# Kernel tuning notes

Hardware: AMD Instinct MI355X
Metric: run time of the kernel (lower is better)

The kernel has to match this reference:

```python
import jax, jax.numpy as jnp
import numpy as np

BLOCK = 128      # ModelArgs.block_size
FP8_MAX = 448.0  # e4m3 max, used by act_quant


def setup_inputs() -> dict:
    key = jax.random.key(0)
    k1, k2, k3 = jax.random.split(key, 3)
    M, K, O = 8192, 4096, 4096
    x = jax.random.normal(k1, (M, K), dtype=jnp.float32)
    # 'fp8' weight values (simulated in fp32) and blockwise fp32 scales
    weight = jax.random.normal(k2, (O, K), dtype=jnp.float32)
    w_scale = jax.random.uniform(k3, (O // BLOCK, K // BLOCK), dtype=jnp.float32,
                                 minval=0.5, maxval=1.5)
    return {"x": x, "weight": weight, "w_scale": w_scale}


def reference(x, weight, w_scale):
    M, K = x.shape
    O = weight.shape[0]
    Kb, Ob = K // BLOCK, O // BLOCK

    # --- act_quant: per-(row, k-block) scale = amax/448, quantized vals x/scale ---
    xb = x.reshape(M, Kb, BLOCK)
    sx = jnp.max(jnp.abs(xb), axis=-1, keepdims=True) / FP8_MAX  # [M, Kb, 1]
    xq = xb / sx                                                  # simulated fp8 activations

    # --- weight_dequant: blockwise scale expansion ---
    wdq = (weight.reshape(Ob, BLOCK, Kb, BLOCK) * w_scale[:, None, :, None]).reshape(O, K)

    # --- fp8_gemm: y = (xq * sx) @ wdq^T  (activation scales folded back per block) ---
    xd = (xq * sx).reshape(M, K)
    y = jnp.einsum('mk,ok->mo', xd, wdq)  # [M, O]
    return y
```

## Files before the change

### kernel.cpp

```cpp
#include <hip/hip_runtime.h>

#define M_DIM 8192
#define K_DIM 4096
#define O_DIM 4096
#define QB    128
#define BK    64
#define BMT   256
#define BNT   256

typedef __attribute__((ext_vector_type(8))) short  short8;
typedef __attribute__((ext_vector_type(4))) float  floatx4;

#define AS1 __attribute__((address_space(1)))
#define AS3 __attribute__((address_space(3)))

__device__ __forceinline__ short f2bf(float f) {
    unsigned u = __float_as_uint(f);
    unsigned r = u + 0x7fffu + ((u >> 16) & 1u);
    return (short)(r >> 16);
}

__global__ __launch_bounds__(512) void cvt_fused(const float* __restrict__ x,
                                                 const float* __restrict__ w,
                                                 const float* __restrict__ s,
                                                 short* __restrict__ xb,
                                                 short* __restrict__ wb) {
    const size_t NX = (size_t)M_DIM * K_DIM / 8;
    size_t t = (size_t)blockIdx.x * 512 + threadIdx.x;
    if (t < NX) {
        size_t i = t * 8;
        floatx4 f0 = *(const floatx4*)(x + i);
        floatx4 f1 = *(const floatx4*)(x + i + 4);
        short8 o;
        o[0] = f2bf(f0[0]); o[1] = f2bf(f0[1]); o[2] = f2bf(f0[2]); o[3] = f2bf(f0[3]);
        o[4] = f2bf(f1[0]); o[5] = f2bf(f1[1]); o[6] = f2bf(f1[2]); o[7] = f2bf(f1[3]);
        *(short8*)(xb + i) = o;
    } else {
        size_t i = (t - NX) * 8;
        int o = (int)(i >> 12);
        int k = (int)(i & (K_DIM - 1));
        float sc = s[(o >> 7) * (K_DIM / QB) + (k >> 7)];
        floatx4 f0 = *(const floatx4*)(w + i);
        floatx4 f1 = *(const floatx4*)(w + i + 4);
        short8 v;
        v[0] = f2bf(f0[0] * sc); v[1] = f2bf(f0[1] * sc);
        v[2] = f2bf(f0[2] * sc); v[3] = f2bf(f0[3] * sc);
        v[4] = f2bf(f1[0] * sc); v[5] = f2bf(f1[1] * sc);
        v[6] = f2bf(f1[2] * sc); v[7] = f2bf(f1[3] * sc);
        *(short8*)(wb + i) = v;
    }
}

#define WLG12 asm volatile("s_waitcnt lgkmcnt(12)" ::: "memory")
#define WLG8  asm volatile("s_waitcnt lgkmcnt(8)" ::: "memory")
#define WLG0  asm volatile("s_waitcnt lgkmcnt(0)" ::: "memory")
#define WVM2  asm volatile("s_waitcnt vmcnt(2)" ::: "memory")
#define WVM0  asm volatile("s_waitcnt vmcnt(0)" ::: "memory")
#define BARR  __builtin_amdgcn_s_barrier()
#define SCHEDB __builtin_amdgcn_sched_barrier(0)
#define SP1   __builtin_amdgcn_s_setprio(1)
#define SP0   __builtin_amdgcn_s_setprio(0)

#define LDA4(DST, BUF, ROFF)                                                    \
    _Pragma("unroll")                                                           \
    for (int mi = 0; mi < 4; ++mi) {                                            \
        DST[mi][0] = *(const short8*)&lsA[BUF][rA + (ROFF) + mi * 1024 + pc0];  \
        DST[mi][1] = *(const short8*)&lsA[BUF][rA + (ROFF) + mi * 1024 + pc1];  \
    }

#define LDB2(DST, BUF, ROFF)                                                    \
    _Pragma("unroll")                                                           \
    for (int ni = 0; ni < 2; ++ni) {                                            \
        DST[ni][0] = *(const short8*)&lsB[BUF][rB + (ROFF) + ni * 1024 + pc0];  \
        DST[ni][1] = *(const short8*)&lsB[BUF][rB + (ROFF) + ni * 1024 + pc1];  \
    }

#define RDA0(B) LDA4(a0, B, 0)
#define RDA1(B) LDA4(a1, B, 4096)
#define RDB0(B) LDB2(b0, B, 0)
#define RDB1(B) LDB2(b1, B, 2048)

#define MM16(AF, BF, MO, NO)                                                    \
    _Pragma("unroll")                                                           \
    for (int mi = 0; mi < 4; ++mi)                                              \
        _Pragma("unroll")                                                       \
        for (int ni = 0; ni < 2; ++ni)                                          \
            _Pragma("unroll")                                                   \
            for (int ks = 0; ks < 2; ++ks)                                      \
                acc[(MO) + mi][(NO) + ni] = __builtin_amdgcn_mfma_f32_16x16x32_bf16( \
                    AF[mi][ks], BF[ni][ks], acc[(MO) + mi][(NO) + ni], 0, 0, 0);

#define STAGE(LS, BUF, GP, KOFF, H)                                             \
    __builtin_amdgcn_global_load_lds(                                           \
        (const AS1 void*)((GP) + (size_t)((H) * 128) * K_DIM + (KOFF)),         \
        (AS3 void*)&LS[BUF][(H) * 128 * BK + dst], 16, 0, 0);                   \
    __builtin_amdgcn_global_load_lds(                                           \
        (const AS1 void*)((GP) + (size_t)((H) * 128 + 64) * K_DIM + (KOFF)),    \
        (AS3 void*)&LS[BUF][((H) * 128 + 64) * BK + dst], 16, 0, 0);

#define PH(STAGES, WAITM, MFMAS)                                                \
    STAGES                                                                      \
    BARR; WAITM; SCHEDB;                                                        \
    SP1;                                                                        \
    MFMAS                                                                       \
    SP0;                                                                        \
    BARR; SCHEDB;

#define PH3(STAGES, VMW, READS, MFMAS)                                          \
    STAGES                                                                      \
    VMW; BARR; SCHEDB;                                                          \
    READS                                                                       \
    WLG12; SCHEDB;                                                              \
    SP1;                                                                        \
    MFMAS                                                                       \
    SP0;                                                                        \
    BARR; SCHEDB;

#define TILE(c, n, k1, k2)                                                      \
    RDB1(c); RDA1(c);                                                           \
    PH(STAGE(lsA, n, gA, k1, 1), WLG12, MM16(a0, b0, 0, 0))                     \
    PH(STAGE(lsB, n, gB, k1, 0), WLG8,  MM16(a0, b1, 0, 2))                     \
    PH(STAGE(lsB, n, gB, k1, 1), WLG0,  MM16(a1, b0, 4, 0))                     \
    PH3(STAGE(lsA, c, gA, k2, 0), WVM2, RDA0(n); RDB0(n);, MM16(a1, b1, 4, 2))

__global__ __launch_bounds__(512, 2) void gemm_bt(const short* __restrict__ A,
                                                  const short* __restrict__ B,
                                                  float* __restrict__ C) {
    __shared__ __align__(16) short lsA[2][BMT * BK];
    __shared__ __align__(16) short lsB[2][BNT * BK];

    const int tid  = threadIdx.x;
    const int lane = tid & 63;
    const int wave = tid >> 6;
    const int wr   = wave >> 2;
    const int wc   = wave & 3;

    const int id  = blockIdx.x;
    const int xcd = id & 7;
    const int j   = id >> 3;
    const int bm  = j >> 1;
    const int bn  = (xcd << 1) | (j & 1);

    const int sr  = tid >> 3;
    const int csw = ((tid & 7) ^ (sr & 7)) << 3;
    const int dst = tid * 8;
    const short* gA = A + (size_t)(bm * BMT + sr) * K_DIM + csw;
    const short* gB = B + (size_t)(bn * BNT + sr) * K_DIM + csw;

    const int frow = lane & 15;
    const int fc   = lane >> 4;
    const int fsw  = frow & 7;
    const int pc0  = (fc ^ fsw) << 3;
    const int pc1  = ((4 + fc) ^ fsw) << 3;
    const int rA   = (wr * 128 + frow) * BK;
    const int rB   = (wc * 64 + frow) * BK;

    floatx4 acc[8][4];
#pragma unroll
    for (int mi = 0; mi < 8; ++mi)
#pragma unroll
        for (int ni = 0; ni < 4; ++ni)
            acc[mi][ni] = (floatx4){0.f, 0.f, 0.f, 0.f};

    short8 a0[4][2], a1[4][2], b0[2][2], b1[2][2];

    STAGE(lsA, 0, gA, 0, 0)
    STAGE(lsA, 0, gA, 0, 1)
    STAGE(lsB, 0, gB, 0, 0)
    STAGE(lsB, 0, gB, 0, 1)
    STAGE(lsA, 1, gA, 64, 0)
    WVM2; BARR; SCHEDB;
    RDA0(0); RDB0(0);

#pragma unroll 1
    for (int it = 0; it < 31; ++it) {
        TILE(0, 1, 64, 128)
        TILE(1, 0, 128, 192)
        gA += 128;
        gB += 128;
    }

    RDB1(0); RDA1(0);
    PH(STAGE(lsA, 1, gA, 64, 1), WLG12, MM16(a0, b0, 0, 0))
    PH(STAGE(lsB, 1, gB, 64, 0), WLG8,  MM16(a0, b1, 0, 2))
    PH(STAGE(lsB, 1, gB, 64, 1), WLG0,  MM16(a1, b0, 4, 0))
    PH3(, WVM0, RDA0(1); RDB0(1);, MM16(a1, b1, 4, 2))

    RDB1(1); RDA1(1);
    PH(, WLG12, MM16(a0, b0, 0, 0))
    PH(, WLG8,  MM16(a0, b1, 0, 2))
    PH(, WLG0,  MM16(a1, b0, 4, 0))
    SCHEDB; SP1; MM16(a1, b1, 4, 2) SP0;

    const int quad  = lane >> 4;
    const int crow0 = bm * BMT + wr * 128 + quad * 4;
    const int ccol0 = bn * BNT + wc * 64 + frow;
#pragma unroll
    for (int mi = 0; mi < 8; ++mi)
#pragma unroll
        for (int ni = 0; ni < 4; ++ni) {
            float* cp = C + (size_t)(crow0 + mi * 16) * O_DIM + (ccol0 + ni * 16);
#pragma unroll
            for (int r = 0; r < 4; ++r)
                __builtin_nontemporal_store(acc[mi][ni][r], cp + (size_t)r * O_DIM);
        }
}

extern "C" void kernel_launch(void* const* d_in, const int* in_sizes, int n_in,
                              void* d_out, int out_size, void* d_ws, size_t ws_size,
                              hipStream_t stream) {
    const float* x  = (const float*)d_in[0];
    const float* w  = (const float*)d_in[1];
    const float* ws = (const float*)d_in[2];
    float* out = (float*)d_out;

    short* xb = (short*)d_ws;
    short* wb = xb + (size_t)M_DIM * K_DIM;

    const size_t total_t = ((size_t)M_DIM * K_DIM + (size_t)O_DIM * K_DIM) / 8;
    cvt_fused<<<(unsigned)(total_t / 512), 512, 0, stream>>>(x, w, ws, xb, wb);

    gemm_bt<<<(M_DIM / BMT) * (O_DIM / BNT), 512, 0, stream>>>(xb, wb, out);
}
```

Measured before the change: 509.9 us.

## Load B fragments directly from global into registers, bypass LDS for B

```diff
diff --git a/kernel.cpp b/kernel.cpp
--- a/kernel.cpp
+++ b/kernel.cpp
@@ -51,11 +51,10 @@
     }
 }
 
-#define WLG12 asm volatile("s_waitcnt lgkmcnt(12)" ::: "memory")
-#define WLG8  asm volatile("s_waitcnt lgkmcnt(8)" ::: "memory")
 #define WLG0  asm volatile("s_waitcnt lgkmcnt(0)" ::: "memory")
-#define WVM2  asm volatile("s_waitcnt vmcnt(2)" ::: "memory")
-#define WVM0  asm volatile("s_waitcnt vmcnt(0)" ::: "memory")
+#define WVM12 asm volatile("s_waitcnt vmcnt(12)" ::: "memory")
+#define WVM8  asm volatile("s_waitcnt vmcnt(8)" ::: "memory")
+#define WVM4  asm volatile("s_waitcnt vmcnt(4)" ::: "memory")
 #define BARR  __builtin_amdgcn_s_barrier()
 #define SCHEDB __builtin_amdgcn_sched_barrier(0)
 #define SP1   __builtin_amdgcn_s_setprio(1)
@@ -68,19 +67,18 @@
         DST[mi][1] = *(const short8*)&lsA[BUF][rA + (ROFF) + mi * 1024 + pc1];  \
     }
 
-#define LDB2(DST, BUF, ROFF)                                                    \
-    _Pragma("unroll")                                                           \
-    for (int ni = 0; ni < 2; ++ni) {                                            \
-        DST[ni][0] = *(const short8*)&lsB[BUF][rB + (ROFF) + ni * 1024 + pc0];  \
-        DST[ni][1] = *(const short8*)&lsB[BUF][rB + (ROFF) + ni * 1024 + pc1];  \
-    }
-
 #define RDA0(B) LDA4(a0, B, 0)
 #define RDA1(B) LDA4(a1, B, 4096)
-#define RDB0(B) LDB2(b0, B, 0)
-#define RDB1(B) LDB2(b1, B, 2048)
-
-#define MM16(AF, BF, MO, NO)                                                    \
+
+#define ISSUE_B(DST, KOFF)                                                      \
+    _Pragma("unroll")                                                           \
+    for (int ni = 0; ni < 4; ++ni)                                              \
+        _Pragma("unroll")                                                       \
+        for (int ks = 0; ks < 2; ++ks)                                          \
+            DST[ni][ks] = *(const short8*)(gBF + (size_t)ni * 16 * K_DIM +      \
+                                           (KOFF) + ks * 32);
+
+#define MMQ(AF, BB, NB, MO, NO)                                                 \
     _Pragma("unroll")                                                           \
     for (int mi = 0; mi < 4; ++mi)                                              \
         _Pragma("unroll")                                                       \
@@ -88,46 +86,32 @@
             _Pragma("unroll")                                                   \
             for (int ks = 0; ks < 2; ++ks)                                      \
                 acc[(MO) + mi][(NO) + ni] = __builtin_amdgcn_mfma_f32_16x16x32_bf16( \
-                    AF[mi][ks], BF[ni][ks], acc[(MO) + mi][(NO) + ni], 0, 0, 0);
-
-#define STAGE(LS, BUF, GP, KOFF, H)                                             \
+                    AF[mi][ks], BB[(NB) + ni][ks], acc[(MO) + mi][(NO) + ni], 0, 0, 0);
+
+#define STAGE(BUF, KOFF, H)                                                     \
     __builtin_amdgcn_global_load_lds(                                           \
-        (const AS1 void*)((GP) + (size_t)((H) * 128) * K_DIM + (KOFF)),         \
-        (AS3 void*)&LS[BUF][(H) * 128 * BK + dst], 16, 0, 0);                   \
+        (const AS1 void*)(gA + (size_t)((H) * 128) * K_DIM + (KOFF)),           \
+        (AS3 void*)&lsA[BUF][(H) * 128 * BK + dst], 16, 0, 0);                  \
     __builtin_amdgcn_global_load_lds(                                           \
-        (const AS1 void*)((GP) + (size_t)((H) * 128 + 64) * K_DIM + (KOFF)),    \
-        (AS3 void*)&LS[BUF][((H) * 128 + 64) * BK + dst], 16, 0, 0);
-
-#define PH(STAGES, WAITM, MFMAS)                                                \
-    STAGES                                                                      \
-    BARR; WAITM; SCHEDB;                                                        \
-    SP1;                                                                        \
-    MFMAS                                                                       \
-    SP0;                                                                        \
-    BARR; SCHEDB;
-
-#define PH3(STAGES, VMW, READS, MFMAS)                                          \
-    STAGES                                                                      \
-    VMW; BARR; SCHEDB;                                                          \
-    READS                                                                       \
-    WLG12; SCHEDB;                                                              \
-    SP1;                                                                        \
-    MFMAS                                                                       \
-    SP0;                                                                        \
-    BARR; SCHEDB;
-
-#define TILE(c, n, k1, k2)                                                      \
-    RDB1(c); RDA1(c);                                                           \
-    PH(STAGE(lsA, n, gA, k1, 1), WLG12, MM16(a0, b0, 0, 0))                     \
-    PH(STAGE(lsB, n, gB, k1, 0), WLG8,  MM16(a0, b1, 0, 2))                     \
-    PH(STAGE(lsB, n, gB, k1, 1), WLG0,  MM16(a1, b0, 4, 0))                     \
-    PH3(STAGE(lsA, c, gA, k2, 0), WVM2, RDA0(n); RDB0(n);, MM16(a1, b1, 4, 2))
+        (const AS1 void*)(gA + (size_t)((H) * 128 + 64) * K_DIM + (KOFF)),      \
+        (AS3 void*)&lsA[BUF][((H) * 128 + 64) * BK + dst], 16, 0, 0);
+
+#define TILE(c, n, BC, BN, KB, KA)                                              \
+    RDA1(c);                                                                    \
+    SP1; MMQ(a0, BC, 0, 0, 0) MMQ(a0, BC, 2, 0, 2) SP0;                         \
+    ISSUE_B(BN, KB)                                                             \
+    WLG0; BARR; SCHEDB;                                                         \
+    STAGE(c, KA, 0)                                                             \
+    SP1; MMQ(a1, BC, 0, 4, 0) SP0;                                              \
+    STAGE(c, KA, 1)                                                             \
+    SP1; MMQ(a1, BC, 2, 4, 2) SP0;                                              \
+    WVM12; BARR; SCHEDB;                                                        \
+    RDA0(n);
 
 __global__ __launch_bounds__(512, 2) void gemm_bt(const short* __restrict__ A,
                                                   const short* __restrict__ B,
                                                   float* __restrict__ C) {
     __shared__ __align__(16) short lsA[2][BMT * BK];
-    __shared__ __align__(16) short lsB[2][BNT * BK];
 
     const int tid  = threadIdx.x;
     const int lane = tid & 63;
@@ -145,15 +129,15 @@
     const int csw = ((tid & 7) ^ (sr & 7)) << 3;
     const int dst = tid * 8;
     const short* gA = A + (size_t)(bm * BMT + sr) * K_DIM + csw;
-    const short* gB = B + (size_t)(bn * BNT + sr) * K_DIM + csw;
 
     const int frow = lane & 15;
     const int fc   = lane >> 4;
+    const short* gBF = B + (size_t)(bn * BNT + wc * 64 + frow) * K_DIM + fc * 8;
+
     const int fsw  = frow & 7;
     const int pc0  = (fc ^ fsw) << 3;
     const int pc1  = ((4 + fc) ^ fsw) << 3;
     const int rA   = (wr * 128 + frow) * BK;
-    const int rB   = (wc * 64 + frow) * BK;
 
     floatx4 acc[8][4];
 #pragma unroll
@@ -162,35 +146,36 @@
         for (int ni = 0; ni < 4; ++ni)
             acc[mi][ni] = (floatx4){0.f, 0.f, 0.f, 0.f};
 
-    short8 a0[4][2], a1[4][2], b0[2][2], b1[2][2];
-
-    STAGE(lsA, 0, gA, 0, 0)
-    STAGE(lsA, 0, gA, 0, 1)
-    STAGE(lsB, 0, gB, 0, 0)
-    STAGE(lsB, 0, gB, 0, 1)
-    STAGE(lsA, 1, gA, 64, 0)
-    WVM2; BARR; SCHEDB;
-    RDA0(0); RDB0(0);
+    short8 a0[4][2], a1[4][2], bA[4][2], bB[4][2];
+
+    ISSUE_B(bA, 0)
+    STAGE(0, 0, 0)
+    STAGE(0, 0, 1)
+    STAGE(1, 64, 0)
+    STAGE(1, 64, 1)
+    WVM4; BARR; SCHEDB;
+    RDA0(0);
 
 #pragma unroll 1
     for (int it = 0; it < 31; ++it) {
-        TILE(0, 1, 64, 128)
-        TILE(1, 0, 128, 192)
-        gA += 128;
-        gB += 128;
+        TILE(0, 1, bA, bB, 64, 128)
+        TILE(1, 0, bB, bA, 128, 192)
+        gA  += 128;
+        gBF += 128;
     }
 
-    RDB1(0); RDA1(0);
-    PH(STAGE(lsA, 1, gA, 64, 1), WLG12, MM16(a0, b0, 0, 0))
-    PH(STAGE(lsB, 1, gB, 64, 0), WLG8,  MM16(a0, b1, 0, 2))
-    PH(STAGE(lsB, 1, gB, 64, 1), WLG0,  MM16(a1, b0, 4, 0))
-    PH3(, WVM0, RDA0(1); RDB0(1);, MM16(a1, b1, 4, 2))
-
-    RDB1(1); RDA1(1);
-    PH(, WLG12, MM16(a0, b0, 0, 0))
-    PH(, WLG8,  MM16(a0, b1, 0, 2))
-    PH(, WLG0,  MM16(a1, b0, 4, 0))
-    SCHEDB; SP1; MM16(a1, b1, 4, 2) SP0;
+    RDA1(0);
+    SP1; MMQ(a0, bA, 0, 0, 0) MMQ(a0, bA, 2, 0, 2) SP0;
+    ISSUE_B(bB, 64)
+    WLG0; BARR; SCHEDB;
+    SP1; MMQ(a1, bA, 0, 4, 0) MMQ(a1, bA, 2, 4, 2) SP0;
+    WVM8; BARR; SCHEDB;
+    RDA0(1);
+
+    RDA1(1);
+    SP1; MMQ(a0, bB, 0, 0, 0) MMQ(a0, bB, 2, 0, 2) SP0;
+    WLG0;
+    SP1; MMQ(a1, bB, 0, 4, 0) MMQ(a1, bB, 2, 4, 2) SP0;
 
     const int quad  = lane >> 4;
     const int crow0 = bm * BMT + wr * 128 + quad * 4;
@@ -202,7 +187,7 @@
             float* cp = C + (size_t)(crow0 + mi * 16) * O_DIM + (ccol0 + ni * 16);
 #pragma unroll
             for (int r = 0; r < 4; ++r)
-                __builtin_nontemporal_store(acc[mi][ni][r], cp + (size_t)r * O_DIM);
+                cp[(size_t)r * O_DIM] = acc[mi][ni][r];
         }
 }
 
```

After: 590.5 us. +15.8%, slower.
